# Performance work log

Hardware: AMD Instinct MI355X
Metric: run time of the kernel (lower is better)

Reference implementation:

```python
import jax, jax.numpy as jnp
import numpy as np

NUM_HEADS = 12


def setup_inputs() -> dict:
    key = jax.random.key(0)
    k1, k2, k3 = jax.random.split(key, 3)
    B, S, D = 8, 1024, 768
    x = jax.random.normal(k1, (B, S, D), dtype=jnp.float32)
    # Linear weights, torch convention [out_features, in_features], small init
    w_qkv = jax.random.normal(k2, (3 * D, D), dtype=jnp.float32) * 0.02
    b_qkv = jnp.zeros((3 * D,), dtype=jnp.float32)
    w_proj = jax.random.normal(k3, (D, D), dtype=jnp.float32) * 0.02
    b_proj = jnp.zeros((D,), dtype=jnp.float32)
    return {"x": x, "w_qkv": w_qkv, "b_qkv": b_qkv, "w_proj": w_proj, "b_proj": b_proj}


def reference(x, w_qkv, b_qkv, w_proj, b_proj):
    B, S, D = x.shape
    H = NUM_HEADS
    hd = D // H
    qkv = x @ w_qkv.T + b_qkv                      # [B, S, 3D]
    qkv = qkv.reshape(B, S, 3, H, hd).transpose(2, 0, 3, 1, 4)  # [3, B, H, S, hd]
    q, k, v = qkv[0], qkv[1], qkv[2]
    # NOTE: source computes self.scale but never applies it -> unscaled QK^T
    weights = jnp.einsum('bhqd,bhkd->bhqk', q, k)  # [B, H, S, S]
    attn = jax.nn.softmax(weights, axis=-1)        # dropout = 0 (eval)
    out = jnp.einsum('bhqk,bhkd->bhqd', attn, v)   # [B, H, S, hd]
    out = out.transpose(0, 2, 1, 3).reshape(B, S, D)
    return out @ w_proj.T + b_proj
```

## Files before the change

kernel.cpp:

```cpp
#include <hip/hip_runtime.h>


typedef short bf16x8 __attribute__((ext_vector_type(8)));
typedef float f32x4  __attribute__((ext_vector_type(4)));

#define MFMA16(a, b, c) __builtin_amdgcn_mfma_f32_16x16x32_bf16((a), (b), (c), 0, 0, 0)

__device__ __forceinline__ unsigned short f2bf(float f) {
    union { float f; unsigned int u; } v; v.f = f;
    unsigned int u = v.u;
    return (unsigned short)((u + 0x7fffu + ((u >> 16) & 1u)) >> 16);
}

__device__ __forceinline__ unsigned int cvt2(float x, float y) {
#if __has_builtin(__builtin_amdgcn_cvt_pk_bf16_f32)
    auto v = __builtin_amdgcn_cvt_pk_bf16_f32(x, y);
    unsigned int b; __builtin_memcpy(&b, &v, 4); return b;
#else
    return (unsigned int)f2bf(x) | ((unsigned int)f2bf(y) << 16);
#endif
}

__device__ __forceinline__ void gl2lds16(const unsigned short* g, unsigned short* l) {
    __builtin_amdgcn_global_load_lds(
        (const unsigned int __attribute__((address_space(1)))*)g,
        (unsigned int __attribute__((address_space(3)))*)l,
        16, 0, 0);
}

__global__ void cvt3_kernel(const float* __restrict__ x,
                            const float* __restrict__ wq,
                            const float* __restrict__ wp,
                            unsigned short* __restrict__ xb,
                            unsigned short* __restrict__ wqb,
                            unsigned short* __restrict__ wpb) {
    int i = blockIdx.x * 256 + threadIdx.x;
    const float* s; unsigned short* d; int off;
    if (i < 1572864)      { s = x;  d = xb;  off = i; }
    else if (i < 2015232) { s = wq; d = wqb; off = i - 1572864; }
    else                  { s = wp; d = wpb; off = i - 2015232; }
    float4 v = ((const float4*)s)[off];
    ushort4 o;
    o.x = f2bf(v.x); o.y = f2bf(v.y); o.z = f2bf(v.z); o.w = f2bf(v.w);
    ((ushort4*)d)[off] = o;
}

__global__ __launch_bounds__(256) void gemm_qkv(
    const unsigned short* __restrict__ A,
    const unsigned short* __restrict__ Bm,
    const float* __restrict__ bias,
    unsigned short* __restrict__ Qo,
    unsigned short* __restrict__ Ko,
    unsigned short* __restrict__ Vto) {
    const int K = 768;
    __shared__ __align__(16) unsigned short smem[16384];
    const int tid = threadIdx.x;
    const int wave = tid >> 6, lane = tid & 63;
    const int quad = lane >> 4, l16 = lane & 15;
    const int wm = (wave >> 1) * 64, wn = (wave & 1) * 64;
    const int tileM = blockIdx.x * 128, tileN = blockIdx.y * 128;

    f32x4 zero4 = {0.f, 0.f, 0.f, 0.f};
    f32x4 acc[4][4];
#pragma unroll
    for (int i = 0; i < 4; ++i)
#pragma unroll
        for (int j = 0; j < 4; ++j) acc[i][j] = zero4;

    const unsigned short* Ab = A + (size_t)tileM * K;
    const unsigned short* Bb = Bm + (size_t)tileN * K;

    auto stage = [&](int k0, int buf) {
        unsigned short* Ad = smem + buf * 4096;
        unsigned short* Bd = smem + 8192 + buf * 4096;
#pragma unroll
        for (int i = 0; i < 2; ++i) {
            int s = tid + (i << 8);
            int r = s >> 2, c = s & 3;
            int dst = ((wave << 6) + (i << 8)) * 8;
            gl2lds16(Ab + (size_t)r * K + k0 + c * 8, Ad + dst);
            gl2lds16(Bb + (size_t)r * K + k0 + c * 8, Bd + dst);
        }
    };

    stage(0, 0);
    for (int it = 0; it < 24; ++it) {
        __syncthreads();
        if (it + 1 < 24) stage((it + 1) << 5, (it + 1) & 1);
        const unsigned short* Ar = smem + (it & 1) * 4096;
        const unsigned short* Br = smem + 8192 + (it & 1) * 4096;
        bf16x8 af[4], bfr[4];
#pragma unroll
        for (int t = 0; t < 4; ++t) {
            af[t]  = *(const bf16x8*)(Ar + (wm + t * 16 + l16) * 32 + quad * 8);
            bfr[t] = *(const bf16x8*)(Br + (wn + t * 16 + l16) * 32 + quad * 8);
        }
#pragma unroll
        for (int tm = 0; tm < 4; ++tm)
#pragma unroll
            for (int tn = 0; tn < 4; ++tn)
                acc[tm][tn] = MFMA16(af[tm], bfr[tn], acc[tm][tn]);
    }

    const int t = blockIdx.y / 6;
    if (t < 2) {
        const float scale = (t == 0) ? 1.44269504f : 1.0f;
        unsigned short* dst = (t == 0) ? Qo : Ko;
        const int nb = tileN - t * 768 + wn;
#pragma unroll
        for (int tm = 0; tm < 4; ++tm) {
#pragma unroll
            for (int tn = 0; tn < 4; ++tn) {
                int nl = nb + tn * 16 + l16;
                float bv = bias[tileN + wn + tn * 16 + l16];
#pragma unroll
                for (int r = 0; r < 4; ++r) {
                    int m = tileM + wm + tm * 16 + quad * 4 + r;
                    dst[(size_t)m * 768 + nl] = f2bf((acc[tm][tn][r] + bv) * scale);
                }
            }
        }
    } else {
        const int b = tileM >> 10, srow = tileM & 1023;
#pragma unroll
        for (int h2 = 0; h2 < 2; ++h2) {
            __syncthreads();
            if ((wn >> 6) == h2) {
#pragma unroll
                for (int tn = 0; tn < 4; ++tn) {
                    int dl = tn * 16 + l16;
                    float bv = bias[tileN + wn + dl];
#pragma unroll
                    for (int tm = 0; tm < 4; ++tm) {
                        int mb = wm + tm * 16 + quad * 4;
                        uint2 pk;
                        pk.x = cvt2(acc[tm][tn][0] + bv, acc[tm][tn][1] + bv);
                        pk.y = cvt2(acc[tm][tn][2] + bv, acc[tm][tn][3] + bv);
                        *(uint2*)(smem + dl * 136 + mb) = pk;
                    }
                }
            }
            __syncthreads();
#pragma unroll
            for (int pass = 0; pass < 4; ++pass) {
                int dl = pass * 16 + (tid >> 4), soff = (tid & 15) * 8;
                bf16x8 row = *(const bf16x8*)(smem + dl * 136 + soff);
                int rem = tileN + h2 * 64 + dl - 1536;
                int h = rem >> 6, d = rem & 63;
                *(bf16x8*)(Vto + (((size_t)b * 12 + h) * 64 + d) * 1024 + srow + soff) = row;
            }
        }
    }
}

__global__ __launch_bounds__(256) void attn_kernel(
    const unsigned short* __restrict__ Q,
    const unsigned short* __restrict__ Kg,
    const unsigned short* __restrict__ Vt,
    unsigned short* __restrict__ O) {
    __shared__ __align__(16) unsigned short smem[24576];
    unsigned short* Ps = smem;

    const int tid = threadIdx.x;
    const int wave = tid >> 6, lane = tid & 63;
    const int quad = lane >> 4, l16 = lane & 15;
    const int s4 = l16 & 3;
    const int qt = blockIdx.x;
    const int bh = blockIdx.y;
    const int b = bh / 12, h = bh - b * 12;

    const unsigned short* Qb = Q  + ((size_t)b * 1024 + qt * 128) * 768 + h * 64;
    const unsigned short* Kb = Kg + (size_t)b * 1024 * 768 + h * 64;
    const unsigned short* Vb = Vt + (size_t)bh * 64 * 1024;

    auto stageKV = [&](int kv0, int buf) {
        int r = tid >> 2, c = tid & 3;
        const unsigned short* gk = Kb + (size_t)(kv0 + r) * 768 + c * 8;
        const unsigned short* gv = Vb + (size_t)r * 1024 + kv0 + c * 8;
        unsigned short* Kd = smem + 8192 + buf * 4096;
        unsigned short* Vd = smem + 16384 + buf * 4096;
        int dst = (wave << 6) * 8;
        gl2lds16(gk,      Kd + dst);
        gl2lds16(gk + 32, Kd + 2048 + dst);
        gl2lds16(gv,      Vd + dst);
        gl2lds16(gv + 32, Vd + 2048 + dst);
    };

#pragma unroll
    for (int i = 0; i < 2; ++i) {
        int s = tid + (i << 8);
        int r = s >> 2, c = s & 3;
        const unsigned short* gq = Qb + (size_t)r * 768 + c * 8;
        int dst = ((wave << 6) + (i << 8)) * 8;
        gl2lds16(gq,      smem + dst);
        gl2lds16(gq + 32, smem + 4096 + dst);
    }
    stageKV(0, 0);
    __syncthreads();
    bf16x8 qf[2][2];
#pragma unroll
    for (int ks = 0; ks < 2; ++ks)
#pragma unroll
        for (int tq = 0; tq < 2; ++tq)
            qf[ks][tq] = *(const bf16x8*)(smem + ks * 4096 +
                                          (wave * 32 + tq * 16 + l16) * 32 + quad * 8);
    __syncthreads();

    f32x4 zero4 = {0.f, 0.f, 0.f, 0.f};
    f32x4 oacc[2][4];
    float rsum[2] = {0.f, 0.f};
#pragma unroll
    for (int tm = 0; tm < 2; ++tm)
#pragma unroll
        for (int tv = 0; tv < 4; ++tv) oacc[tm][tv] = zero4;

    for (int it = 0; it < 16; ++it) {
        if (it + 1 < 16) stageKV((it + 1) << 6, (it + 1) & 1);
        const unsigned short* Kr = smem + 8192 + (it & 1) * 4096;
        const unsigned short* Vr = smem + 16384 + (it & 1) * 4096;

        f32x4 st[4][2];
#pragma unroll
        for (int tk = 0; tk < 4; ++tk)
#pragma unroll
            for (int tq = 0; tq < 2; ++tq) st[tk][tq] = zero4;
#pragma unroll
        for (int ks = 0; ks < 2; ++ks) {
            bf16x8 kf[4];
#pragma unroll
            for (int tk = 0; tk < 4; ++tk)
                kf[tk] = *(const bf16x8*)(Kr + ks * 2048 + (tk * 16 + l16) * 32 + quad * 8);
#pragma unroll
            for (int tk = 0; tk < 4; ++tk)
#pragma unroll
                for (int tq = 0; tq < 2; ++tq)
                    st[tk][tq] = MFMA16(kf[tk], qf[ks][tq], st[tk][tq]);
        }

#pragma unroll
        for (int tq = 0; tq < 2; ++tq) {
            unsigned short* prp = Ps + (wave * 32 + tq * 16 + l16) * 64 + quad * 4;
#pragma unroll
            for (int tk = 0; tk < 4; ++tk) {
                float e0 = __builtin_amdgcn_exp2f(st[tk][tq][0]);
                float e1 = __builtin_amdgcn_exp2f(st[tk][tq][1]);
                float e2 = __builtin_amdgcn_exp2f(st[tk][tq][2]);
                float e3 = __builtin_amdgcn_exp2f(st[tk][tq][3]);
                rsum[tq] += (e0 + e1) + (e2 + e3);
                uint2 pk;
                pk.x = cvt2(e0, e1);
                pk.y = cvt2(e2, e3);
                *(uint2*)(prp + ((tk ^ s4) << 4)) = pk;
            }
        }

#pragma unroll
        for (int ks2 = 0; ks2 < 2; ++ks2) {
            bf16x8 ap[2], bv[4];
            int colswz = ((ks2 << 5) + (quad << 3)) ^ (s4 << 4);
#pragma unroll
            for (int tm = 0; tm < 2; ++tm)
                ap[tm] = *(const bf16x8*)(Ps + (wave * 32 + tm * 16 + l16) * 64 + colswz);
#pragma unroll
            for (int tv = 0; tv < 4; ++tv)
                bv[tv] = *(const bf16x8*)(Vr + ks2 * 2048 + (tv * 16 + l16) * 32 + quad * 8);
#pragma unroll
            for (int tm = 0; tm < 2; ++tm)
#pragma unroll
                for (int tv = 0; tv < 4; ++tv)
                    oacc[tm][tv] = MFMA16(ap[tm], bv[tv], oacc[tm][tv]);
        }
        __syncthreads();
    }

#pragma unroll
    for (int tq = 0; tq < 2; ++tq) {
        rsum[tq] += __shfl_xor(rsum[tq], 16, 64);
        rsum[tq] += __shfl_xor(rsum[tq], 32, 64);
    }
    float* sums = (float*)smem;
    if (quad == 0) {
        sums[wave * 32 + l16]      = rsum[0];
        sums[wave * 32 + 16 + l16] = rsum[1];
    }
    __syncthreads();

#pragma unroll
    for (int tm = 0; tm < 2; ++tm) {
        f32x4 inv;
#pragma unroll
        for (int r = 0; r < 4; ++r)
            inv[r] = 1.0f / sums[wave * 32 + tm * 16 + quad * 4 + r];
#pragma unroll
        for (int tv = 0; tv < 4; ++tv)
#pragma unroll
            for (int r = 0; r < 4; ++r) {
                int srow = qt * 128 + wave * 32 + tm * 16 + quad * 4 + r;
                int col = h * 64 + tv * 16 + l16;
                O[((size_t)b * 1024 + srow) * 768 + col] = f2bf(oacc[tm][tv][r] * inv[r]);
            }
    }
}

__global__ __launch_bounds__(256) void gemm_proj(
    const unsigned short* __restrict__ A,
    const unsigned short* __restrict__ Bm,
    const float* __restrict__ bias,
    float* __restrict__ out) {
    const int K = 768;
    __shared__ __align__(16) unsigned short smem[16384];
    const int tid = threadIdx.x;
    const int wave = tid >> 6, lane = tid & 63;
    const int quad = lane >> 4, l16 = lane & 15;
    const int wm = (wave >> 1) * 64, wn = (wave & 1) * 64;
    const int tileM = blockIdx.x * 128, tileN = blockIdx.y * 128;

    f32x4 zero4 = {0.f, 0.f, 0.f, 0.f};
    f32x4 acc[4][4];
#pragma unroll
    for (int i = 0; i < 4; ++i)
#pragma unroll
        for (int j = 0; j < 4; ++j) acc[i][j] = zero4;

    const unsigned short* Ab = A + (size_t)tileM * K;
    const unsigned short* Bb = Bm + (size_t)tileN * K;

    auto stage = [&](int k0, int buf) {
        unsigned short* Ad = smem + buf * 4096;
        unsigned short* Bd = smem + 8192 + buf * 4096;
#pragma unroll
        for (int i = 0; i < 2; ++i) {
            int s = tid + (i << 8);
            int r = s >> 2, c = s & 3;
            int dst = ((wave << 6) + (i << 8)) * 8;
            gl2lds16(Ab + (size_t)r * K + k0 + c * 8, Ad + dst);
            gl2lds16(Bb + (size_t)r * K + k0 + c * 8, Bd + dst);
        }
    };

    stage(0, 0);
    for (int it = 0; it < 24; ++it) {
        __syncthreads();
        if (it + 1 < 24) stage((it + 1) << 5, (it + 1) & 1);
        const unsigned short* Ar = smem + (it & 1) * 4096;
        const unsigned short* Br = smem + 8192 + (it & 1) * 4096;
        bf16x8 af[4], bfr[4];
#pragma unroll
        for (int t = 0; t < 4; ++t) {
            af[t]  = *(const bf16x8*)(Ar + (wm + t * 16 + l16) * 32 + quad * 8);
            bfr[t] = *(const bf16x8*)(Br + (wn + t * 16 + l16) * 32 + quad * 8);
        }
#pragma unroll
        for (int tm = 0; tm < 4; ++tm)
#pragma unroll
            for (int tn = 0; tn < 4; ++tn)
                acc[tm][tn] = MFMA16(af[tm], bfr[tn], acc[tm][tn]);
    }

#pragma unroll
    for (int tm = 0; tm < 4; ++tm) {
#pragma unroll
        for (int tn = 0; tn < 4; ++tn) {
            int n = tileN + wn + tn * 16 + l16;
            float bv = bias[n];
#pragma unroll
            for (int r = 0; r < 4; ++r) {
                int m = tileM + wm + tm * 16 + quad * 4 + r;
                out[(size_t)m * 768 + n] = acc[tm][tn][r] + bv;
            }
        }
    }
}

extern "C" void kernel_launch(void* const* d_in, const int* in_sizes, int n_in,
                              void* d_out, int out_size, void* d_ws, size_t ws_size,
                              hipStream_t stream) {
    (void)in_sizes; (void)n_in; (void)out_size; (void)ws_size;
    const float* x      = (const float*)d_in[0];
    const float* w_qkv  = (const float*)d_in[1];
    const float* b_qkv  = (const float*)d_in[2];
    const float* w_proj = (const float*)d_in[3];
    const float* b_proj = (const float*)d_in[4];
    float* out = (float*)d_out;

    char* ws = (char*)d_ws;
    unsigned short* xb     = (unsigned short*)(ws + 0);
    unsigned short* wqkvb  = (unsigned short*)(ws + 12582912);
    unsigned short* wprojb = (unsigned short*)(ws + 16121856);
    unsigned short* Qw     = (unsigned short*)(ws + 17301504);
    unsigned short* Kw     = (unsigned short*)(ws + 29884416);
    unsigned short* Vtw    = (unsigned short*)(ws + 42467328);

    cvt3_kernel<<<8448, 256, 0, stream>>>(x, w_qkv, w_proj, xb, wqkvb, wprojb);
    gemm_qkv<<<dim3(64, 18), 256, 0, stream>>>(xb, wqkvb, b_qkv, Qw, Kw, Vtw);
    attn_kernel<<<dim3(8, 96), 256, 0, stream>>>(Qw, Kw, Vtw, xb);
    gemm_proj<<<dim3(64, 6), 256, 0, stream>>>(xb, wprojb, b_proj, out);
}
```

Before: 200.0 us.

## Use 512-thread single-buffered GEMM blocks with smaller per-wave tiles

Both GEMM kernels now run with 8 waves per block instead of 4. Each wave computes a 32x64 sub-tile instead of 64x64, which halves the accumulator registers and raises occupancy. The LDS double buffering is replaced by a single buffer with two barriers per k-step, which cuts shared memory use so more blocks fit per CU. In exchange, loads are no longer overlapped with MFMA inside a block, and the kernel relies on other resident waves to hide that latency. The V-transpose epilogue is adjusted to the new wave layout.

```diff
diff --git a/kernel.cpp b/kernel.cpp
--- a/kernel.cpp
+++ b/kernel.cpp
@@ -45,7 +45,7 @@
     ((ushort4*)d)[off] = o;
 }
 
-__global__ __launch_bounds__(256) void gemm_qkv(
+__global__ __launch_bounds__(512, 4) void gemm_qkv(
     const unsigned short* __restrict__ A,
     const unsigned short* __restrict__ Bm,
     const float* __restrict__ bias,
@@ -53,53 +53,44 @@
     unsigned short* __restrict__ Ko,
     unsigned short* __restrict__ Vto) {
     const int K = 768;
-    __shared__ __align__(16) unsigned short smem[16384];
+    __shared__ __align__(16) unsigned short smem[8704];
+    unsigned short* As = smem;
+    unsigned short* Bs = smem + 4096;
     const int tid = threadIdx.x;
     const int wave = tid >> 6, lane = tid & 63;
     const int quad = lane >> 4, l16 = lane & 15;
-    const int wm = (wave >> 1) * 64, wn = (wave & 1) * 64;
+    const int wm = (wave >> 1) * 32, wn = (wave & 1) * 64;
     const int tileM = blockIdx.x * 128, tileN = blockIdx.y * 128;
 
     f32x4 zero4 = {0.f, 0.f, 0.f, 0.f};
-    f32x4 acc[4][4];
-#pragma unroll
-    for (int i = 0; i < 4; ++i)
+    f32x4 acc[2][4];
+#pragma unroll
+    for (int i = 0; i < 2; ++i)
 #pragma unroll
         for (int j = 0; j < 4; ++j) acc[i][j] = zero4;
 
-    const unsigned short* Ab = A + (size_t)tileM * K;
-    const unsigned short* Bb = Bm + (size_t)tileN * K;
-
-    auto stage = [&](int k0, int buf) {
-        unsigned short* Ad = smem + buf * 4096;
-        unsigned short* Bd = smem + 8192 + buf * 4096;
-#pragma unroll
-        for (int i = 0; i < 2; ++i) {
-            int s = tid + (i << 8);
-            int r = s >> 2, c = s & 3;
-            int dst = ((wave << 6) + (i << 8)) * 8;
-            gl2lds16(Ab + (size_t)r * K + k0 + c * 8, Ad + dst);
-            gl2lds16(Bb + (size_t)r * K + k0 + c * 8, Bd + dst);
-        }
-    };
-
-    stage(0, 0);
-    for (int it = 0; it < 24; ++it) {
-        __syncthreads();
-        if (it + 1 < 24) stage((it + 1) << 5, (it + 1) & 1);
-        const unsigned short* Ar = smem + (it & 1) * 4096;
-        const unsigned short* Br = smem + 8192 + (it & 1) * 4096;
-        bf16x8 af[4], bfr[4];
-#pragma unroll
-        for (int t = 0; t < 4; ++t) {
-            af[t]  = *(const bf16x8*)(Ar + (wm + t * 16 + l16) * 32 + quad * 8);
-            bfr[t] = *(const bf16x8*)(Br + (wn + t * 16 + l16) * 32 + quad * 8);
-        }
-#pragma unroll
-        for (int tm = 0; tm < 4; ++tm)
+    const int sr = tid >> 2, sc = tid & 3;
+    const unsigned short* Ag = A + (size_t)(tileM + sr) * K + sc * 8;
+    const unsigned short* Bg = Bm + (size_t)(tileN + sr) * K + sc * 8;
+    const int sdst = wave << 9;
+
+    for (int k0 = 0; k0 < K; k0 += 32) {
+        gl2lds16(Ag + k0, As + sdst);
+        gl2lds16(Bg + k0, Bs + sdst);
+        __syncthreads();
+        bf16x8 af[2], bfr[4];
+#pragma unroll
+        for (int t = 0; t < 2; ++t)
+            af[t] = *(const bf16x8*)(As + (wm + t * 16 + l16) * 32 + quad * 8);
+#pragma unroll
+        for (int t = 0; t < 4; ++t)
+            bfr[t] = *(const bf16x8*)(Bs + (wn + t * 16 + l16) * 32 + quad * 8);
+#pragma unroll
+        for (int tm = 0; tm < 2; ++tm)
 #pragma unroll
             for (int tn = 0; tn < 4; ++tn)
                 acc[tm][tn] = MFMA16(af[tm], bfr[tn], acc[tm][tn]);
+        __syncthreads();
     }
 
     const int t = blockIdx.y / 6;
@@ -108,7 +99,7 @@
         unsigned short* dst = (t == 0) ? Qo : Ko;
         const int nb = tileN - t * 768 + wn;
 #pragma unroll
-        for (int tm = 0; tm < 4; ++tm) {
+        for (int tm = 0; tm < 2; ++tm) {
 #pragma unroll
             for (int tn = 0; tn < 4; ++tn) {
                 int nl = nb + tn * 16 + l16;
@@ -125,13 +116,13 @@
 #pragma unroll
         for (int h2 = 0; h2 < 2; ++h2) {
             __syncthreads();
-            if ((wn >> 6) == h2) {
+            if ((wave & 1) == h2) {
 #pragma unroll
                 for (int tn = 0; tn < 4; ++tn) {
                     int dl = tn * 16 + l16;
-                    float bv = bias[tileN + wn + dl];
-#pragma unroll
-                    for (int tm = 0; tm < 4; ++tm) {
+                    float bv = bias[tileN + h2 * 64 + dl];
+#pragma unroll
+                    for (int tm = 0; tm < 2; ++tm) {
                         int mb = wm + tm * 16 + quad * 4;
                         uint2 pk;
                         pk.x = cvt2(acc[tm][tn][0] + bv, acc[tm][tn][1] + bv);
@@ -142,8 +133,8 @@
             }
             __syncthreads();
 #pragma unroll
-            for (int pass = 0; pass < 4; ++pass) {
-                int dl = pass * 16 + (tid >> 4), soff = (tid & 15) * 8;
+            for (int pass = 0; pass < 2; ++pass) {
+                int dl = pass * 32 + (tid >> 4), soff = (tid & 15) * 8;
                 bf16x8 row = *(const bf16x8*)(smem + dl * 136 + soff);
                 int rem = tileN + h2 * 64 + dl - 1536;
                 int h = rem >> 6, d = rem & 63;
@@ -302,63 +293,54 @@
     }
 }
 
-__global__ __launch_bounds__(256) void gemm_proj(
+__global__ __launch_bounds__(512, 4) void gemm_proj(
     const unsigned short* __restrict__ A,
     const unsigned short* __restrict__ Bm,
     const float* __restrict__ bias,
     float* __restrict__ out) {
     const int K = 768;
-    __shared__ __align__(16) unsigned short smem[16384];
+    __shared__ __align__(16) unsigned short smem[8192];
+    unsigned short* As = smem;
+    unsigned short* Bs = smem + 4096;
     const int tid = threadIdx.x;
     const int wave = tid >> 6, lane = tid & 63;
     const int quad = lane >> 4, l16 = lane & 15;
-    const int wm = (wave >> 1) * 64, wn = (wave & 1) * 64;
+    const int wm = (wave >> 1) * 32, wn = (wave & 1) * 64;
     const int tileM = blockIdx.x * 128, tileN = blockIdx.y * 128;
 
     f32x4 zero4 = {0.f, 0.f, 0.f, 0.f};
-    f32x4 acc[4][4];
-#pragma unroll
-    for (int i = 0; i < 4; ++i)
+    f32x4 acc[2][4];
+#pragma unroll
+    for (int i = 0; i < 2; ++i)
 #pragma unroll
         for (int j = 0; j < 4; ++j) acc[i][j] = zero4;
 
-    const unsigned short* Ab = A + (size_t)tileM * K;
-    const unsigned short* Bb = Bm + (size_t)tileN * K;
-
-    auto stage = [&](int k0, int buf) {
-        unsigned short* Ad = smem + buf * 4096;
-        unsigned short* Bd = smem + 8192 + buf * 4096;
-#pragma unroll
-        for (int i = 0; i < 2; ++i) {
-            int s = tid + (i << 8);
-            int r = s >> 2, c = s & 3;
-            int dst = ((wave << 6) + (i << 8)) * 8;
-            gl2lds16(Ab + (size_t)r * K + k0 + c * 8, Ad + dst);
-            gl2lds16(Bb + (size_t)r * K + k0 + c * 8, Bd + dst);
-        }
-    };
-
-    stage(0, 0);
-    for (int it = 0; it < 24; ++it) {
-        __syncthreads();
-        if (it + 1 < 24) stage((it + 1) << 5, (it + 1) & 1);
-        const unsigned short* Ar = smem + (it & 1) * 4096;
-        const unsigned short* Br = smem + 8192 + (it & 1) * 4096;
-        bf16x8 af[4], bfr[4];
-#pragma unroll
-        for (int t = 0; t < 4; ++t) {
-            af[t]  = *(const bf16x8*)(Ar + (wm + t * 16 + l16) * 32 + quad * 8);
-            bfr[t] = *(const bf16x8*)(Br + (wn + t * 16 + l16) * 32 + quad * 8);
-        }
-#pragma unroll
-        for (int tm = 0; tm < 4; ++tm)
+    const int sr = tid >> 2, sc = tid & 3;
+    const unsigned short* Ag = A + (size_t)(tileM + sr) * K + sc * 8;
+    const unsigned short* Bg = Bm + (size_t)(tileN + sr) * K + sc * 8;
+    const int sdst = wave << 9;
+
+    for (int k0 = 0; k0 < K; k0 += 32) {
+        gl2lds16(Ag + k0, As + sdst);
+        gl2lds16(Bg + k0, Bs + sdst);
+        __syncthreads();
+        bf16x8 af[2], bfr[4];
+#pragma unroll
+        for (int t = 0; t < 2; ++t)
+            af[t] = *(const bf16x8*)(As + (wm + t * 16 + l16) * 32 + quad * 8);
+#pragma unroll
+        for (int t = 0; t < 4; ++t)
+            bfr[t] = *(const bf16x8*)(Bs + (wn + t * 16 + l16) * 32 + quad * 8);
+#pragma unroll
+        for (int tm = 0; tm < 2; ++tm)
 #pragma unroll
             for (int tn = 0; tn < 4; ++tn)
                 acc[tm][tn] = MFMA16(af[tm], bfr[tn], acc[tm][tn]);
-    }
-
-#pragma unroll
-    for (int tm = 0; tm < 4; ++tm) {
+        __syncthreads();
+    }
+
+#pragma unroll
+    for (int tm = 0; tm < 2; ++tm) {
 #pragma unroll
         for (int tn = 0; tn < 4; ++tn) {
             int n = tileN + wn + tn * 16 + l16;
@@ -392,7 +374,7 @@
     unsigned short* Vtw    = (unsigned short*)(ws + 42467328);
 
     cvt3_kernel<<<8448, 256, 0, stream>>>(x, w_qkv, w_proj, xb, wqkvb, wprojb);
-    gemm_qkv<<<dim3(64, 18), 256, 0, stream>>>(xb, wqkvb, b_qkv, Qw, Kw, Vtw);
+    gemm_qkv<<<dim3(64, 18), 512, 0, stream>>>(xb, wqkvb, b_qkv, Qw, Kw, Vtw);
     attn_kernel<<<dim3(8, 96), 256, 0, stream>>>(Qw, Kw, Vtw, xb);
-    gemm_proj<<<dim3(64, 6), 256, 0, stream>>>(xb, wprojb, b_proj, out);
-}
+    gemm_proj<<<dim3(64, 6), 512, 0, stream>>>(xb, wprojb, b_proj, out);
+}
```

Result: slower. 207.9 us (+4.0%).
